# Kernel optimization log

Hardware: AMD Instinct MI355X
Metric: run time of the kernel (lower is better)

Reference implementation:

```python
import jax, jax.numpy as jnp
from jax import lax
import numpy as np

B, T, M, AUX, H, OUT = 256, 256, 8, 32, 64, 1

def setup_inputs() -> dict:
    key = jax.random.key(0)
    ks = jax.random.split(key, 12)
    s_aux = 1.0 / np.sqrt(AUX)
    s_h = 1.0 / np.sqrt(H)
    return {
        "x_m": jax.random.uniform(ks[0], (B, T, M), dtype=jnp.float32),
        "x_a": jax.random.normal(ks[1], (B, T, AUX), dtype=jnp.float32),
        # junction: aux -> (M, H) logits, softmax over H (outgoing mass fractions)
        "Wj": jax.random.uniform(ks[2], (AUX, M * H), jnp.float32, -s_aux, s_aux),
        "bj": jnp.zeros((M * H,), jnp.float32),
        # redistribution: aux -> (H, H) logits, softmax over last dim
        "Wr": jax.random.uniform(ks[3], (AUX, H * H), jnp.float32, -s_aux, s_aux),
        "br": jnp.zeros((H * H,), jnp.float32),
        # out gate: sigmoid(Linear(aux))
        "Wo": jax.random.uniform(ks[4], (AUX, H), jnp.float32, -s_aux, s_aux),
        "bo": jnp.zeros((H,), jnp.float32),
        # final fc: hidden -> out_size
        "Wfc": jax.random.uniform(ks[5], (H, OUT), jnp.float32, -s_h, s_h),
        "bfc": jnp.zeros((OUT,), jnp.float32),
    }


def reference(x_m, x_a, Wj, bj, Wr, br, Wo, bo, Wfc, bfc):
    Bb = x_m.shape[0]

    def step(c, xs):
        xm, xa = xs  # [B, M], [B, AUX]
        j = jax.nn.softmax((xa @ Wj + bj).reshape(Bb, M, H), axis=-1)
        r = jax.nn.softmax((xa @ Wr + br).reshape(Bb, H, H), axis=-1)
        o = jax.nn.sigmoid(xa @ Wo + bo)
        m_in = jnp.einsum('bm,bmh->bh', xm, j)   # inflow distributed to cells
        m_sys = jnp.einsum('bh,bhk->bk', c, r)   # internal redistribution
        m_new = m_in + m_sys
        return m_new, o * m_new                  # (new cell state, output)

    c0 = jnp.zeros((Bb, H), dtype=x_m.dtype)
    xs = (jnp.swapaxes(x_m, 0, 1), jnp.swapaxes(x_a, 0, 1))  # time-major
    c_final, a = lax.scan(step, c0, xs)          # a: [T, B, H]
    out = a[-1] @ Wfc + bfc                      # fc on last timestep output
    return out, c_final
```

## Files before the change

kernel.cpp:

```cpp
#include <hip/hip_runtime.h>


namespace {

constexpr int B_ = 256, T_ = 256, M_ = 8, AUX_ = 32, H_ = 64;
constexpr int NTILE = 288;
constexpr float LOG2E = 1.4426950408889634f;

typedef __fp16 f16x2 __attribute__((ext_vector_type(2)));
typedef __fp16 f16x8 __attribute__((ext_vector_type(8)));
typedef float  f32x4 __attribute__((ext_vector_type(4)));
typedef int    i32x4 __attribute__((ext_vector_type(4)));

union V8 { f16x8 v; f16x2 p[4]; i32x4 i; };

#if __has_builtin(__builtin_amdgcn_exp2f)
#define EXP2(x) __builtin_amdgcn_exp2f(x)
#else
#define EXP2(x) exp2f(x)
#endif

#define MFMA16(A, Bv, C) __builtin_amdgcn_mfma_f32_16x16x32_f16((A), (Bv), (C), 0, 0, 0)

__device__ __forceinline__ float dot2(f16x2 a, f16x2 b, float c) {
    return __builtin_amdgcn_fdot2(a, b, c, false);
}

template <int CTRL>
__device__ __forceinline__ float dpp_add(float v) {
    int t = __builtin_amdgcn_update_dpp(0, __builtin_bit_cast(int, v),
                                        CTRL, 0xf, 0xf, true);
    return v + __builtin_bit_cast(float, t);
}
__device__ __forceinline__ float sum16_all(float v) {
    v = dpp_add<0xB1>(v);
    v = dpp_add<0x4E>(v);
    v = dpp_add<0x141>(v);
    v = dpp_add<0x140>(v);
    return v;
}
__device__ __forceinline__ float sum64_uni(float v) {
    v = dpp_add<0x111>(v); v = dpp_add<0x112>(v); v = dpp_add<0x114>(v);
    v = dpp_add<0x118>(v); v = dpp_add<0x142>(v); v = dpp_add<0x143>(v);
    return __builtin_bit_cast(float,
        __builtin_amdgcn_readlane(__builtin_bit_cast(int, v), 63));
}

__device__ __forceinline__ int pack_pair_rne(float v) {
    const int hv = (int)__builtin_bit_cast(unsigned short, (__fp16)v);
    const int ev = __builtin_amdgcn_update_dpp(0, hv, 0xA0, 0xf, 0xf, true);
    const int ov = __builtin_amdgcn_update_dpp(0, hv, 0xF5, 0xf, 0xf, true);
    return ev | (ov << 16);
}

#define LDS_FENCE() __asm__ volatile("s_waitcnt lgkmcnt(0)" ::: "memory")

__global__ __launch_bounds__(64)
void nomc_prep(const float* __restrict__ Wj, const float* __restrict__ bj,
               const float* __restrict__ Wr, const float* __restrict__ br,
               void* __restrict__ ws)
{
    const int gt = blockIdx.x;
    const int l = threadIdx.x, q = l >> 4, l15 = l & 15;
    const float* src; const float* bsrc; int stride;
    if (gt < 256) { const int n = gt * 16 + l15;        src = Wr + n; bsrc = br + n; stride = 4096; }
    else          { const int n = (gt - 256) * 16 + l15; src = Wj + n; bsrc = bj + n; stride = 512; }
    V8 v;
#pragma unroll
    for (int j = 0; j < 4; ++j) {
        const float f0 = src[(q * 8 + 2 * j)     * stride] * LOG2E;
        const float f1 = src[(q * 8 + 2 * j + 1) * stride] * LOG2E;
        v.p[j] = __builtin_amdgcn_cvt_pkrtz(f0, f1);
    }
    *(i32x4*)((char*)ws + (size_t)gt * 1024 + l * 16) = v.i;
    if (l < 16)
        ((float*)((char*)ws + NTILE * 1024))[gt * 16 + l] = bsrc[0] * LOG2E;
}

__global__ __launch_bounds__(1024, 4)
void nomc_main(const float* __restrict__ x_m, const float* __restrict__ x_a,
               const float* __restrict__ Wo, const float* __restrict__ bo,
               const float* __restrict__ Wfc, const float* __restrict__ bfc,
               const void* __restrict__ ws, float* __restrict__ out)
{
    const int b = blockIdx.x, tid = threadIdx.x;
    const int w = tid >> 6, l = tid & 63, q = l >> 4, l15 = l & 15;

    __shared__ __align__(16) __fp16 RT[16][8][64][8];
    __shared__ __align__(16) __fp16 JT[16][64][8];
    __shared__ float sinv[16][64];
    __shared__ __align__(16) __fp16 xj[16][8];
    __shared__ __align__(16) __fp16 minL[16][64];
    __shared__ float xm_lds[T_][M_];
    __shared__ float cfin_lds[H_];

    {
        const float* xmb = x_m + (size_t)b * T_ * M_;
        for (int i = tid; i < T_ * M_; i += 1024) (&xm_lds[0][0])[i] = xmb[i];
    }
    __syncthreads();

    const int ngrp = (w < 8) ? 5 : 4;
    const int g0   = (w < 8) ? w * 5 : 40 + (w - 8) * 4;
    const char* wsb = (const char*)ws;
    const float* wbias = (const float*)(wsb + NTILE * 1024);

    const int sx = q << 1;

    float c0 = 0.f, c1 = 0.f, c2 = 0.f, c3 = 0.f;

    for (int it = 0; it < 16; ++it) {
        V8 af;
        {
            const float* xa = x_a + ((size_t)b * T_ + it * 16 + l15) * AUX_ + q * 8;
            const f32x4 x0 = *(const f32x4*)xa;
            const f32x4 x1 = *(const f32x4*)(xa + 4);
            af.p[0] = __builtin_amdgcn_cvt_pkrtz(x0.x, x0.y);
            af.p[1] = __builtin_amdgcn_cvt_pkrtz(x0.z, x0.w);
            af.p[2] = __builtin_amdgcn_cvt_pkrtz(x1.x, x1.y);
            af.p[3] = __builtin_amdgcn_cvt_pkrtz(x1.z, x1.w);
        }

        for (int g = 0; g < ngrp; ++g) {
            const int gg = g0 + g;
            float es0 = 0.f, es1 = 0.f, es2 = 0.f, es3 = 0.f;
#pragma unroll
            for (int tt = 0; tt < 4; ++tt) {
                const int gt = gg * 4 + tt;
                V8 bf; bf.i = *(const i32x4*)(wsb + (size_t)gt * 1024 + l * 16);
                const float bv = wbias[gt * 16 + l15];
                f32x4 acc = {bv, bv, bv, bv};
                acc = MFMA16(af.v, bf.v, acc);
                const float e0 = EXP2(acc[0]), e1 = EXP2(acc[1]);
                const float e2 = EXP2(acc[2]), e3 = EXP2(acc[3]);
                const int kk = (tt << 4) + l15;
                if (gg < 64) {
                    const int hb = gg >> 3, p = (gg & 7) ^ sx;
                    RT[q * 4 + 0][hb][kk][p] = (__fp16)e0;
                    RT[q * 4 + 1][hb][kk][p] = (__fp16)e1;
                    RT[q * 4 + 2][hb][kk][p] = (__fp16)e2;
                    RT[q * 4 + 3][hb][kk][p] = (__fp16)e3;
                } else {
                    const int mp = (gg - 64) ^ sx;
                    JT[q * 4 + 0][kk][mp] = (__fp16)e0;
                    JT[q * 4 + 1][kk][mp] = (__fp16)e1;
                    JT[q * 4 + 2][kk][mp] = (__fp16)e2;
                    JT[q * 4 + 3][kk][mp] = (__fp16)e3;
                }
                es0 += e0; es1 += e1; es2 += e2; es3 += e3;
            }
            const float sr0 = sum16_all(es0), sr1 = sum16_all(es1);
            const float sr2 = sum16_all(es2), sr3 = sum16_all(es3);
            if (l15 == 0) {
                if (gg < 64) {
                    sinv[q * 4 + 0][gg] = __builtin_amdgcn_rcpf(sr0);
                    sinv[q * 4 + 1][gg] = __builtin_amdgcn_rcpf(sr1);
                    sinv[q * 4 + 2][gg] = __builtin_amdgcn_rcpf(sr2);
                    sinv[q * 4 + 3][gg] = __builtin_amdgcn_rcpf(sr3);
                } else {
                    const int m = (gg - 64) ^ sx;
                    xj[q * 4 + 0][m] = (__fp16)(xm_lds[it * 16 + q * 4 + 0][gg - 64] * __builtin_amdgcn_rcpf(sr0));
                    xj[q * 4 + 1][m] = (__fp16)(xm_lds[it * 16 + q * 4 + 1][gg - 64] * __builtin_amdgcn_rcpf(sr1));
                    xj[q * 4 + 2][m] = (__fp16)(xm_lds[it * 16 + q * 4 + 2][gg - 64] * __builtin_amdgcn_rcpf(sr2));
                    xj[q * 4 + 3][m] = (__fp16)(xm_lds[it * 16 + q * 4 + 3][gg - 64] * __builtin_amdgcn_rcpf(sr3));
                }
            }
        }
        __syncthreads();

        {
            V8 jv; jv.v = *(const f16x8*)&JT[w][l][0];
            V8 xv; xv.v = *(const f16x8*)&xj[w][0];
            float s = 0.f;
            s = dot2(jv.p[0], xv.p[0], s);
            s = dot2(jv.p[1], xv.p[1], s);
            s = dot2(jv.p[2], xv.p[2], s);
            s = dot2(jv.p[3], xv.p[3], s);
            minL[w][l] = (__fp16)s;
        }
        __syncthreads();

        if (w == 15) {
            const int ab = q << 5;
            for (int u = 0; u < 16; ++u) {
                const int sig = (u >> 2) & 3;
                const float mi0 = (float)minL[u][l15];
                const float mi1 = (float)minL[u][16 + l15];
                const float mi2 = (float)minL[u][32 + l15];
                const float mi3 = (float)minL[u][48 + l15];
                const float svl = sinv[u][l];
                V8 b00, b01, b10, b11, b20, b21, b30, b31;
                b00.v = *(const f16x8*)&RT[u][q][l15][0];
                b01.v = *(const f16x8*)&RT[u][4 + q][l15][0];
                b10.v = *(const f16x8*)&RT[u][q][16 + l15][0];
                b11.v = *(const f16x8*)&RT[u][4 + q][16 + l15][0];
                b20.v = *(const f16x8*)&RT[u][q][32 + l15][0];
                b21.v = *(const f16x8*)&RT[u][4 + q][32 + l15][0];
                b30.v = *(const f16x8*)&RT[u][q][48 + l15][0];
                b31.v = *(const f16x8*)&RT[u][4 + q][48 + l15][0];
                const float cown = (q == 0) ? c0 : (q == 1) ? c1 : (q == 2) ? c2 : c3;
                const int spk = pack_pair_rne(cown * svl);
                V8 A0f, A1f;
                A0f.i[0] = __builtin_amdgcn_ds_bpermute(ab + ((0 ^ sig) << 3), spk);
                A0f.i[1] = __builtin_amdgcn_ds_bpermute(ab + ((1 ^ sig) << 3), spk);
                A0f.i[2] = __builtin_amdgcn_ds_bpermute(ab + ((2 ^ sig) << 3), spk);
                A0f.i[3] = __builtin_amdgcn_ds_bpermute(ab + ((3 ^ sig) << 3), spk);
                A1f.i[0] = __builtin_amdgcn_ds_bpermute(128 + ab + ((0 ^ sig) << 3), spk);
                A1f.i[1] = __builtin_amdgcn_ds_bpermute(128 + ab + ((1 ^ sig) << 3), spk);
                A1f.i[2] = __builtin_amdgcn_ds_bpermute(128 + ab + ((2 ^ sig) << 3), spk);
                A1f.i[3] = __builtin_amdgcn_ds_bpermute(128 + ab + ((3 ^ sig) << 3), spk);
                f32x4 a0 = {mi0, mi0, mi0, mi0};
                a0 = MFMA16(A0f.v, b00.v, a0);
                a0 = MFMA16(A1f.v, b01.v, a0);
                f32x4 a1 = {mi1, mi1, mi1, mi1};
                a1 = MFMA16(A0f.v, b10.v, a1);
                a1 = MFMA16(A1f.v, b11.v, a1);
                f32x4 a2 = {mi2, mi2, mi2, mi2};
                a2 = MFMA16(A0f.v, b20.v, a2);
                a2 = MFMA16(A1f.v, b21.v, a2);
                f32x4 a3 = {mi3, mi3, mi3, mi3};
                a3 = MFMA16(A0f.v, b30.v, a3);
                a3 = MFMA16(A1f.v, b31.v, a3);
                c0 = a0[0]; c1 = a1[0]; c2 = a2[0]; c3 = a3[0];
            }
        }
        __syncthreads();
    }

    if (w == 15) {
        const float cown = (q == 0) ? c0 : (q == 1) ? c1 : (q == 2) ? c2 : c3;
        cfin_lds[l] = cown;
        LDS_FENCE();
        const float* xa = x_a + ((size_t)b * T_ + (T_ - 1)) * AUX_;
        float L = bo[l];
#pragma unroll
        for (int a = 0; a < AUX_; ++a) L = fmaf(xa[a], Wo[a * H_ + l], L);
        const float o = 1.0f / (1.0f + __expf(-L));
        const float cfin = cfin_lds[l];
        float p = (o * cfin) * Wfc[l];
        p = sum64_uni(p);
        if (l == 0) out[b] = p + bfc[0];
        out[B_ + b * H_ + l] = cfin;
    }
}

}

extern "C" void kernel_launch(void* const* d_in, const int* in_sizes, int n_in,
                              void* d_out, int out_size, void* d_ws, size_t ws_size,
                              hipStream_t stream) {
    const float* x_m = (const float*)d_in[0];
    const float* x_a = (const float*)d_in[1];
    const float* Wj  = (const float*)d_in[2];
    const float* bj  = (const float*)d_in[3];
    const float* Wr  = (const float*)d_in[4];
    const float* br  = (const float*)d_in[5];
    const float* Wo  = (const float*)d_in[6];
    const float* bo  = (const float*)d_in[7];
    const float* Wfc = (const float*)d_in[8];
    const float* bfc = (const float*)d_in[9];
    float* out = (float*)d_out;

    hipLaunchKernelGGL(nomc_prep, dim3(NTILE), dim3(64), 0, stream,
                       Wj, bj, Wr, br, d_ws);
    hipLaunchKernelGGL(nomc_main, dim3(B_), dim3(1024), 0, stream,
                       x_m, x_a, Wo, bo, Wfc, bfc, d_ws, out);
}
```

Baseline: 247.0 us.

## Balance softmax tile work evenly across all 16 waves and prefetch weight tiles

Replaces the uneven 5/4 group-per-wave split of the 72 logit groups with a balanced scheme. Each wave now does 4 redistribution groups, and the 8 junction groups are split so that a pair of waves each handles two of the four tiles. Partial softmax sums are combined through a small shared array and an extra barrier. All weight tiles and biases are loaded into registers up front so the global loads can overlap the MFMA/exp work. The cost is one extra __syncthreads per chunk and higher register pressure from holding 18 tiles per wave.

Measured after the change: 367.8 us. +48.9%, slower.

```diff
diff --git a/kernel.cpp b/kernel.cpp
--- a/kernel.cpp
+++ b/kernel.cpp
@@ -93,6 +93,7 @@
     __shared__ __align__(16) __fp16 minL[16][64];
     __shared__ float xm_lds[T_][M_];
     __shared__ float cfin_lds[H_];
+    __shared__ float ph[16][16];
 
     {
         const float* xmb = x_m + (size_t)b * T_ * M_;
@@ -100,10 +101,10 @@
     }
     __syncthreads();
 
-    const int ngrp = (w < 8) ? 5 : 4;
-    const int g0   = (w < 8) ? w * 5 : 40 + (w - 8) * 4;
     const char* wsb = (const char*)ws;
     const float* wbias = (const float*)(wsb + NTILE * 1024);
+    const int a_sh = w >> 1;
+    const int tb = (w & 1) ? 2 : 0;
 
     const int sx = q << 1;
 
@@ -121,49 +122,89 @@
             af.p[3] = __builtin_amdgcn_cvt_pkrtz(x1.z, x1.w);
         }
 
-        for (int g = 0; g < ngrp; ++g) {
-            const int gg = g0 + g;
-            float es0 = 0.f, es1 = 0.f, es2 = 0.f, es3 = 0.f;
+        V8 tj[2]; float bvj[2];
+#pragma unroll
+        for (int s = 0; s < 2; ++s) {
+            const int gt = (64 + a_sh) * 4 + tb + s;
+            tj[s].i = *(const i32x4*)(wsb + (size_t)gt * 1024 + l * 16);
+            bvj[s] = wbias[gt * 16 + l15];
+        }
+        V8 tr[4][4]; float bvr[4][4];
+#pragma unroll
+        for (int g = 0; g < 4; ++g) {
 #pragma unroll
             for (int tt = 0; tt < 4; ++tt) {
-                const int gt = gg * 4 + tt;
-                V8 bf; bf.i = *(const i32x4*)(wsb + (size_t)gt * 1024 + l * 16);
-                const float bv = wbias[gt * 16 + l15];
+                const int gt = (w * 4 + g) * 4 + tt;
+                tr[g][tt].i = *(const i32x4*)(wsb + (size_t)gt * 1024 + l * 16);
+                bvr[g][tt] = wbias[gt * 16 + l15];
+            }
+        }
+
+        {
+            float ej0 = 0.f, ej1 = 0.f, ej2 = 0.f, ej3 = 0.f;
+#pragma unroll
+            for (int s = 0; s < 2; ++s) {
+                const int tt = tb + s;
+                const float bv = bvj[s];
                 f32x4 acc = {bv, bv, bv, bv};
-                acc = MFMA16(af.v, bf.v, acc);
+                acc = MFMA16(af.v, tj[s].v, acc);
                 const float e0 = EXP2(acc[0]), e1 = EXP2(acc[1]);
                 const float e2 = EXP2(acc[2]), e3 = EXP2(acc[3]);
                 const int kk = (tt << 4) + l15;
-                if (gg < 64) {
-                    const int hb = gg >> 3, p = (gg & 7) ^ sx;
-                    RT[q * 4 + 0][hb][kk][p] = (__fp16)e0;
-                    RT[q * 4 + 1][hb][kk][p] = (__fp16)e1;
-                    RT[q * 4 + 2][hb][kk][p] = (__fp16)e2;
-                    RT[q * 4 + 3][hb][kk][p] = (__fp16)e3;
-                } else {
-                    const int mp = (gg - 64) ^ sx;
-                    JT[q * 4 + 0][kk][mp] = (__fp16)e0;
-                    JT[q * 4 + 1][kk][mp] = (__fp16)e1;
-                    JT[q * 4 + 2][kk][mp] = (__fp16)e2;
-                    JT[q * 4 + 3][kk][mp] = (__fp16)e3;
-                }
+                const int mp = a_sh ^ sx;
+                JT[q * 4 + 0][kk][mp] = (__fp16)e0;
+                JT[q * 4 + 1][kk][mp] = (__fp16)e1;
+                JT[q * 4 + 2][kk][mp] = (__fp16)e2;
+                JT[q * 4 + 3][kk][mp] = (__fp16)e3;
+                ej0 += e0; ej1 += e1; ej2 += e2; ej3 += e3;
+            }
+            ej0 = sum16_all(ej0); ej1 = sum16_all(ej1);
+            ej2 = sum16_all(ej2); ej3 = sum16_all(ej3);
+            if (l15 == 0) {
+                ph[w][q * 4 + 0] = ej0;
+                ph[w][q * 4 + 1] = ej1;
+                ph[w][q * 4 + 2] = ej2;
+                ph[w][q * 4 + 3] = ej3;
+            }
+        }
+        __syncthreads();
+
+#pragma unroll
+        for (int g = 0; g < 4; ++g) {
+            const int gg = w * 4 + g;
+            float es0 = 0.f, es1 = 0.f, es2 = 0.f, es3 = 0.f;
+#pragma unroll
+            for (int tt = 0; tt < 4; ++tt) {
+                const float bv = bvr[g][tt];
+                f32x4 acc = {bv, bv, bv, bv};
+                acc = MFMA16(af.v, tr[g][tt].v, acc);
+                const float e0 = EXP2(acc[0]), e1 = EXP2(acc[1]);
+                const float e2 = EXP2(acc[2]), e3 = EXP2(acc[3]);
+                const int kk = (tt << 4) + l15;
+                const int hb = gg >> 3, p = (gg & 7) ^ sx;
+                RT[q * 4 + 0][hb][kk][p] = (__fp16)e0;
+                RT[q * 4 + 1][hb][kk][p] = (__fp16)e1;
+                RT[q * 4 + 2][hb][kk][p] = (__fp16)e2;
+                RT[q * 4 + 3][hb][kk][p] = (__fp16)e3;
                 es0 += e0; es1 += e1; es2 += e2; es3 += e3;
             }
             const float sr0 = sum16_all(es0), sr1 = sum16_all(es1);
             const float sr2 = sum16_all(es2), sr3 = sum16_all(es3);
             if (l15 == 0) {
-                if (gg < 64) {
-                    sinv[q * 4 + 0][gg] = __builtin_amdgcn_rcpf(sr0);
-                    sinv[q * 4 + 1][gg] = __builtin_amdgcn_rcpf(sr1);
-                    sinv[q * 4 + 2][gg] = __builtin_amdgcn_rcpf(sr2);
-                    sinv[q * 4 + 3][gg] = __builtin_amdgcn_rcpf(sr3);
-                } else {
-                    const int m = (gg - 64) ^ sx;
-                    xj[q * 4 + 0][m] = (__fp16)(xm_lds[it * 16 + q * 4 + 0][gg - 64] * __builtin_amdgcn_rcpf(sr0));
-                    xj[q * 4 + 1][m] = (__fp16)(xm_lds[it * 16 + q * 4 + 1][gg - 64] * __builtin_amdgcn_rcpf(sr1));
-                    xj[q * 4 + 2][m] = (__fp16)(xm_lds[it * 16 + q * 4 + 2][gg - 64] * __builtin_amdgcn_rcpf(sr2));
-                    xj[q * 4 + 3][m] = (__fp16)(xm_lds[it * 16 + q * 4 + 3][gg - 64] * __builtin_amdgcn_rcpf(sr3));
-                }
+                sinv[q * 4 + 0][gg] = __builtin_amdgcn_rcpf(sr0);
+                sinv[q * 4 + 1][gg] = __builtin_amdgcn_rcpf(sr1);
+                sinv[q * 4 + 2][gg] = __builtin_amdgcn_rcpf(sr2);
+                sinv[q * 4 + 3][gg] = __builtin_amdgcn_rcpf(sr3);
+            }
+        }
+
+        if ((w & 1) == 0 && l15 == 0) {
+#pragma unroll
+            for (int r = 0; r < 4; ++r) {
+                const int t = q * 4 + r;
+                const float tot = ph[w][t] + ph[w + 1][t];
+                xj[t][a_sh ^ sx] =
+                    (__fp16)(xm_lds[it * 16 + t][a_sh] * __builtin_amdgcn_rcpf(tot));
             }
         }
         __syncthreads();
```

## Overlap junction softmax for next chunk with serial recurrence wave

Applied to the files above, without the earlier changes.

Moves the junction (J) softmax for chunk it+1 into the phase where waves 0-14 previously sat idle while wave 15 ran the serial recurrence, and merges the m_in dot product into the start of the next iteration. This drops one __syncthreads per chunk. It also rebalances R-tile work to exactly 4 groups per wave with no branches. The cost is a prologue, extra live registers for af across the loop, and more code in the idle-wave branch.

Result: faster. 213.9 us (median of 2 runs) (-13.4%).

```diff
diff --git a/kernel.cpp b/kernel.cpp
--- a/kernel.cpp
+++ b/kernel.cpp
@@ -77,6 +77,47 @@
         ((float*)((char*)ws + NTILE * 1024))[gt * 16 + l] = bsrc[0] * LOG2E;
 }
 
+#define AF_LOAD(ITN)                                                         \
+    do {                                                                     \
+        const float* xa_ = x_a + ((size_t)b * T_ + (ITN) * 16 + l15) * AUX_ + q * 8; \
+        const f32x4 x0_ = *(const f32x4*)xa_;                                \
+        const f32x4 x1_ = *(const f32x4*)(xa_ + 4);                          \
+        af.p[0] = __builtin_amdgcn_cvt_pkrtz(x0_.x, x0_.y);                  \
+        af.p[1] = __builtin_amdgcn_cvt_pkrtz(x0_.z, x0_.w);                  \
+        af.p[2] = __builtin_amdgcn_cvt_pkrtz(x1_.x, x1_.y);                  \
+        af.p[3] = __builtin_amdgcn_cvt_pkrtz(x1_.z, x1_.w);                  \
+    } while (0)
+
+#define J_GROUP(ITN)                                                         \
+    do {                                                                     \
+        float ej0 = 0.f, ej1 = 0.f, ej2 = 0.f, ej3 = 0.f;                    \
+        const int mp = w ^ sx;                                               \
+        _Pragma("unroll")                                                    \
+        for (int tt = 0; tt < 4; ++tt) {                                     \
+            const int gt = (64 + w) * 4 + tt;                                \
+            V8 bf; bf.i = *(const i32x4*)(wsb + (size_t)gt * 1024 + l * 16); \
+            const float bv = wbias[gt * 16 + l15];                           \
+            f32x4 acc = {bv, bv, bv, bv};                                    \
+            acc = MFMA16(af.v, bf.v, acc);                                   \
+            const float e0 = EXP2(acc[0]), e1 = EXP2(acc[1]);                \
+            const float e2 = EXP2(acc[2]), e3 = EXP2(acc[3]);                \
+            const int kk = (tt << 4) + l15;                                  \
+            JT[q * 4 + 0][kk][mp] = (__fp16)e0;                              \
+            JT[q * 4 + 1][kk][mp] = (__fp16)e1;                              \
+            JT[q * 4 + 2][kk][mp] = (__fp16)e2;                              \
+            JT[q * 4 + 3][kk][mp] = (__fp16)e3;                              \
+            ej0 += e0; ej1 += e1; ej2 += e2; ej3 += e3;                      \
+        }                                                                    \
+        ej0 = sum16_all(ej0); ej1 = sum16_all(ej1);                          \
+        ej2 = sum16_all(ej2); ej3 = sum16_all(ej3);                          \
+        if (l15 == 0) {                                                      \
+            xj[q * 4 + 0][mp] = (__fp16)(xm_lds[(ITN) * 16 + q * 4 + 0][w] * __builtin_amdgcn_rcpf(ej0)); \
+            xj[q * 4 + 1][mp] = (__fp16)(xm_lds[(ITN) * 16 + q * 4 + 1][w] * __builtin_amdgcn_rcpf(ej1)); \
+            xj[q * 4 + 2][mp] = (__fp16)(xm_lds[(ITN) * 16 + q * 4 + 2][w] * __builtin_amdgcn_rcpf(ej2)); \
+            xj[q * 4 + 3][mp] = (__fp16)(xm_lds[(ITN) * 16 + q * 4 + 3][w] * __builtin_amdgcn_rcpf(ej3)); \
+        }                                                                    \
+    } while (0)
+
 __global__ __launch_bounds__(1024, 4)
 void nomc_main(const float* __restrict__ x_m, const float* __restrict__ x_a,
                const float* __restrict__ Wo, const float* __restrict__ bo,
@@ -100,30 +141,34 @@
     }
     __syncthreads();
 
-    const int ngrp = (w < 8) ? 5 : 4;
-    const int g0   = (w < 8) ? w * 5 : 40 + (w - 8) * 4;
     const char* wsb = (const char*)ws;
     const float* wbias = (const float*)(wsb + NTILE * 1024);
-
     const int sx = q << 1;
 
+    V8 af;
+    AF_LOAD(0);
+    if (w < 8) J_GROUP(0);
+    __syncthreads();
+
     float c0 = 0.f, c1 = 0.f, c2 = 0.f, c3 = 0.f;
 
     for (int it = 0; it < 16; ++it) {
-        V8 af;
         {
-            const float* xa = x_a + ((size_t)b * T_ + it * 16 + l15) * AUX_ + q * 8;
-            const f32x4 x0 = *(const f32x4*)xa;
-            const f32x4 x1 = *(const f32x4*)(xa + 4);
-            af.p[0] = __builtin_amdgcn_cvt_pkrtz(x0.x, x0.y);
-            af.p[1] = __builtin_amdgcn_cvt_pkrtz(x0.z, x0.w);
-            af.p[2] = __builtin_amdgcn_cvt_pkrtz(x1.x, x1.y);
-            af.p[3] = __builtin_amdgcn_cvt_pkrtz(x1.z, x1.w);
+            V8 jv; jv.v = *(const f16x8*)&JT[w][l][0];
+            V8 xv; xv.v = *(const f16x8*)&xj[w][0];
+            float s = 0.f;
+            s = dot2(jv.p[0], xv.p[0], s);
+            s = dot2(jv.p[1], xv.p[1], s);
+            s = dot2(jv.p[2], xv.p[2], s);
+            s = dot2(jv.p[3], xv.p[3], s);
+            minL[w][l] = (__fp16)s;
         }
 
-        for (int g = 0; g < ngrp; ++g) {
-            const int gg = g0 + g;
+#pragma unroll 1
+        for (int g = 0; g < 4; ++g) {
+            const int gg = w * 4 + g;
             float es0 = 0.f, es1 = 0.f, es2 = 0.f, es3 = 0.f;
+            const int hb = gg >> 3, p = (gg & 7) ^ sx;
 #pragma unroll
             for (int tt = 0; tt < 4; ++tt) {
                 const int gt = gg * 4 + tt;
@@ -134,49 +179,20 @@
                 const float e0 = EXP2(acc[0]), e1 = EXP2(acc[1]);
                 const float e2 = EXP2(acc[2]), e3 = EXP2(acc[3]);
                 const int kk = (tt << 4) + l15;
-                if (gg < 64) {
-                    const int hb = gg >> 3, p = (gg & 7) ^ sx;
-                    RT[q * 4 + 0][hb][kk][p] = (__fp16)e0;
-                    RT[q * 4 + 1][hb][kk][p] = (__fp16)e1;
-                    RT[q * 4 + 2][hb][kk][p] = (__fp16)e2;
-                    RT[q * 4 + 3][hb][kk][p] = (__fp16)e3;
-                } else {
-                    const int mp = (gg - 64) ^ sx;
-                    JT[q * 4 + 0][kk][mp] = (__fp16)e0;
-                    JT[q * 4 + 1][kk][mp] = (__fp16)e1;
-                    JT[q * 4 + 2][kk][mp] = (__fp16)e2;
-                    JT[q * 4 + 3][kk][mp] = (__fp16)e3;
-                }
+                RT[q * 4 + 0][hb][kk][p] = (__fp16)e0;
+                RT[q * 4 + 1][hb][kk][p] = (__fp16)e1;
+                RT[q * 4 + 2][hb][kk][p] = (__fp16)e2;
+                RT[q * 4 + 3][hb][kk][p] = (__fp16)e3;
                 es0 += e0; es1 += e1; es2 += e2; es3 += e3;
             }
             const float sr0 = sum16_all(es0), sr1 = sum16_all(es1);
             const float sr2 = sum16_all(es2), sr3 = sum16_all(es3);
             if (l15 == 0) {
-                if (gg < 64) {
-                    sinv[q * 4 + 0][gg] = __builtin_amdgcn_rcpf(sr0);
-                    sinv[q * 4 + 1][gg] = __builtin_amdgcn_rcpf(sr1);
-                    sinv[q * 4 + 2][gg] = __builtin_amdgcn_rcpf(sr2);
-                    sinv[q * 4 + 3][gg] = __builtin_amdgcn_rcpf(sr3);
-                } else {
-                    const int m = (gg - 64) ^ sx;
-                    xj[q * 4 + 0][m] = (__fp16)(xm_lds[it * 16 + q * 4 + 0][gg - 64] * __builtin_amdgcn_rcpf(sr0));
-                    xj[q * 4 + 1][m] = (__fp16)(xm_lds[it * 16 + q * 4 + 1][gg - 64] * __builtin_amdgcn_rcpf(sr1));
-                    xj[q * 4 + 2][m] = (__fp16)(xm_lds[it * 16 + q * 4 + 2][gg - 64] * __builtin_amdgcn_rcpf(sr2));
-                    xj[q * 4 + 3][m] = (__fp16)(xm_lds[it * 16 + q * 4 + 3][gg - 64] * __builtin_amdgcn_rcpf(sr3));
-                }
+                sinv[q * 4 + 0][gg] = __builtin_amdgcn_rcpf(sr0);
+                sinv[q * 4 + 1][gg] = __builtin_amdgcn_rcpf(sr1);
+                sinv[q * 4 + 2][gg] = __builtin_amdgcn_rcpf(sr2);
+                sinv[q * 4 + 3][gg] = __builtin_amdgcn_rcpf(sr3);
             }
-        }
-        __syncthreads();
-
-        {
-            V8 jv; jv.v = *(const f16x8*)&JT[w][l][0];
-            V8 xv; xv.v = *(const f16x8*)&xj[w][0];
-            float s = 0.f;
-            s = dot2(jv.p[0], xv.p[0], s);
-            s = dot2(jv.p[1], xv.p[1], s);
-            s = dot2(jv.p[2], xv.p[2], s);
-            s = dot2(jv.p[3], xv.p[3], s);
-            minL[w][l] = (__fp16)s;
         }
         __syncthreads();
 
@@ -223,6 +239,10 @@
                 a3 = MFMA16(A1f.v, b31.v, a3);
                 c0 = a0[0]; c1 = a1[0]; c2 = a2[0]; c3 = a3[0];
             }
+            if (it < 15) AF_LOAD(it + 1);
+        } else if (it < 15) {
+            AF_LOAD(it + 1);
+            if (w < 8) J_GROUP(it + 1);
         }
         __syncthreads();
     }
```
